# Kernel optimization log

Hardware: AMD Instinct MI355X
Metric: run time of the kernel (lower is better)

## Reference

```python
import jax, jax.numpy as jnp
import numpy as np
import math

D_MODEL = 1024
NUM_HEADS = 16
D_K = D_MODEL // NUM_HEADS
B, NQ, NK = 2, 2048, 2048


def setup_inputs() -> dict:
    key = jax.random.key(0)
    ks = jax.random.split(key, 14)
    s = 1.0 / math.sqrt(D_MODEL)
    inp = {
        "query": jax.random.normal(ks[0], (B, NQ, D_MODEL), jnp.float32),
        "key": jax.random.normal(ks[1], (B, NK, D_MODEL), jnp.float32),
        "value": jax.random.normal(ks[2], (B, NK, D_MODEL), jnp.float32),
        "mask": jax.random.randint(ks[3], (B, NK), 0, 2, jnp.int32),
        "attn_bias": jax.random.normal(ks[4], (B, NQ, NK), jnp.float32),
        "w_q": jax.random.normal(ks[5], (D_MODEL, D_MODEL), jnp.float32) * s,
        "b_q": jnp.zeros((D_MODEL,), jnp.float32),
        "w_k": jax.random.normal(ks[6], (D_MODEL, D_MODEL), jnp.float32) * s,
        "b_k": jnp.zeros((D_MODEL,), jnp.float32),
        "w_v": jax.random.normal(ks[7], (D_MODEL, D_MODEL), jnp.float32) * s,
        "b_v": jnp.zeros((D_MODEL,), jnp.float32),
        "w_o": jax.random.normal(ks[8], (D_MODEL, D_MODEL), jnp.float32) * s,
        "b_o": jnp.zeros((D_MODEL,), jnp.float32),
    }
    return inp


def reference(query, key, value, mask, attn_bias, w_q, b_q, w_k, b_k, w_v, b_v, w_o, b_o):
    # Linear projections (torch Linear: x @ W^T + b), reshape to [B, H, N, d_k]
    def proj(x, w, b, n):
        return (x @ w.T + b).reshape(x.shape[0], n, NUM_HEADS, D_K).transpose(0, 2, 1, 3)

    Q = proj(query, w_q, b_q, query.shape[1])   # [B,H,Nq,dk]
    K = proj(key, w_k, b_k, key.shape[1])       # [B,H,Nk,dk]
    V = proj(value, w_v, b_v, value.shape[1])   # [B,H,Nk,dk]

    scores = jnp.einsum("bhqd,bhkd->bhqk", Q, K) / math.sqrt(D_K)
    scores = scores + attn_bias[:, None, :, :]           # bias broadcast over heads
    pad = (mask[:, None, None, :] == 0)                   # [B,1,1,Nk]
    scores = jnp.where(pad, jnp.float32(-1e9), scores)
    attn = jax.nn.softmax(scores, axis=-1)                # dropout is identity (eval)
    out = jnp.einsum("bhqk,bhkd->bhqd", attn, V)          # [B,H,Nq,dk]
    out = out.transpose(0, 2, 1, 3).reshape(query.shape[0], query.shape[1], D_MODEL)
    return out @ w_o.T + b_o
```

## Files before the change

kernel.cpp:

```cpp
#include <hip/hip_runtime.h>


typedef short bf16x8 __attribute__((ext_vector_type(8)));
typedef short bf16x4 __attribute__((ext_vector_type(4)));
typedef float f32x4 __attribute__((ext_vector_type(4)));
typedef float f32x16 __attribute__((ext_vector_type(16)));
typedef int i32x4 __attribute__((ext_vector_type(4)));
typedef unsigned short u16;
typedef unsigned short u16x8 __attribute__((ext_vector_type(8)));
typedef unsigned short u16x4 __attribute__((ext_vector_type(4)));

#define MFMA16(a, b, c) __builtin_amdgcn_mfma_f32_16x16x32_bf16((a), (b), (c), 0, 0, 0)
#define MFMA32(a, b, c) __builtin_amdgcn_mfma_f32_32x32x16_bf16((a), (b), (c), 0, 0, 0)
#define GLD16(gp, lp)                                                     \
  __builtin_amdgcn_global_load_lds(                                       \
      (const __attribute__((address_space(1))) void*)(gp),                \
      (__attribute__((address_space(3))) void*)(lp), 16, 0, 0)

#define WAITVM_BAR(N) asm volatile("s_waitcnt vmcnt(" #N ")\ns_barrier" ::: "memory")
#define BAR() asm volatile("s_barrier" ::: "memory")

#if __has_builtin(__builtin_amdgcn_exp2f)
#define EXP2(x) __builtin_amdgcn_exp2f(x)
#else
#define EXP2(x) exp2f(x)
#endif

__device__ __forceinline__ u16 f2bf(float f) {
  union { float f; unsigned u; } v; v.f = f;
  return (u16)((v.u + 0x7fffu + ((v.u >> 16) & 1u)) >> 16);
}
__device__ __forceinline__ unsigned pk2(float x, float y) {
  union { float f; unsigned u; } a, b;
  a.f = x; b.f = y;
  return ((a.u + 0x8000u) >> 16) | ((b.u + 0x8000u) & 0xffff0000u);
}
__device__ __forceinline__ void pl32swap(unsigned& a, unsigned& b) {
  asm("v_permlane32_swap_b32 %0, %1" : "+v"(a), "+v"(b));
}

struct ConvDesc { const float* src; u16* dst; int n; };
struct ConvArgs { ConvDesc d[7]; };

__device__ __forceinline__ void biasprep_body(const float* __restrict__ bias,
                                              const int* __restrict__ mask,
                                              u16* __restrict__ out, int i) {
  const int o0 = i * 16;
  const int rowg = o0 >> 11;
  const int b = rowg >> 11;
  const int off = o0 & 2047;
  const int c = off >> 5;
  const int hi = (off >> 4) & 1;
  const float* src = bias + (size_t)rowg * 2048 + c * 32 + hi * 4;
  const int* msk = mask + b * 2048 + c * 32 + hi * 4;
  u16x8 w0 = {}, w1 = {};
#pragma unroll
  for (int t = 0; t < 4; t++) {
    f32x4 v = *(const f32x4*)(src + t * 8);
    i32x4 m = *(const i32x4*)(msk + t * 8);
#pragma unroll
    for (int j = 0; j < 4; j++) {
      u16 val = (m[j] != 0) ? f2bf(v[j] * 1.44269504f) : (u16)0xFF80;
      if (t < 2) w0[t * 4 + j] = val;
      else       w1[(t - 2) * 4 + j] = val;
    }
  }
  *(u16x8*)(out + o0) = w0;
  *(u16x8*)(out + o0 + 8) = w1;
}

__global__ __launch_bounds__(256)
void k_prep(ConvArgs a, const float* __restrict__ bias,
            const int* __restrict__ mask, u16* __restrict__ bout) {
  if (blockIdx.y == 7) {
    biasprep_body(bias, mask, bout, blockIdx.x * 256 + threadIdx.x);
    return;
  }
  ConvDesc cd = a.d[blockIdx.y];
  int i = (blockIdx.x * 256 + threadIdx.x) * 8;
  if (i >= cd.n) return;
  const float4* s = (const float4*)(cd.src + i);
  float4 f0 = s[0], f1 = s[1];
  u16x8 o;
  o[0] = f2bf(f0.x); o[1] = f2bf(f0.y); o[2] = f2bf(f0.z); o[3] = f2bf(f0.w);
  o[4] = f2bf(f1.x); o[5] = f2bf(f1.y); o[6] = f2bf(f1.z); o[7] = f2bf(f1.w);
  *(u16x8*)(cd.dst + i) = o;
}

__global__ __launch_bounds__(256)
void k_biasprep(const float* __restrict__ bias, const int* __restrict__ mask,
                u16* __restrict__ out) {
  biasprep_body(bias, mask, out, blockIdx.x * 256 + threadIdx.x);
}

template <int MF>
__device__ __forceinline__ void gemm_impl(const u16* __restrict__ A,
                                          const u16* __restrict__ Bw,
                                          const float* __restrict__ bias,
                                          void* __restrict__ outp, int mode,
                                          float oscale) {
  __shared__ u16 As[2][MF * 1024];
  __shared__ u16 Bs[2][4096];
  const int tid = threadIdx.x;
  const int lane = tid & 63;
  const int wv = tid >> 6;
  const int wr = wv >> 1, wc = wv & 1;
  const int m0 = blockIdx.y * (MF * 32), n0 = blockIdx.x * 128;

  f32x4 acc[MF][4] = {};

  const int s0 = tid, s1 = 256 + tid;
  const int r0 = s0 >> 2, c0 = (s0 & 3) ^ (r0 & 3);
  const int r1 = s1 >> 2, c1 = (s1 & 3) ^ (r1 & 3);
  const u16* gA0 = A + (size_t)(m0 + r0) * 1024 + c0 * 8;
  const u16* gA1 = A + (size_t)(m0 + r1) * 1024 + c1 * 8;
  const u16* gB0 = Bw + (size_t)(n0 + r0) * 1024 + c0 * 8;
  const u16* gB1 = Bw + (size_t)(n0 + r1) * 1024 + c1 * 8;
  u16* lA0 = &As[0][(tid & ~63) * 8];
  u16* lB0 = &Bs[0][(tid & ~63) * 8];

  GLD16(gA0, lA0);
  if constexpr (MF == 4) GLD16(gA1, lA0 + 2048);
  GLD16(gB0, lB0);
  GLD16(gB1, lB0 + 2048);
  WAITVM_BAR(0);

#define GSTEP(BUF, K0)                                                     \
  {                                                                        \
    const int nk = ((K0) + 32) & 1023;                                     \
    GLD16(gA0 + nk, lA0 + ((BUF) ^ 1) * (MF * 1024));                      \
    if constexpr (MF == 4)                                                 \
      GLD16(gA1 + nk, lA0 + 2048 + ((BUF) ^ 1) * (MF * 1024));             \
    GLD16(gB0 + nk, lB0 + ((BUF) ^ 1) * 4096);                             \
    GLD16(gB1 + nk, lB0 + 2048 + ((BUF) ^ 1) * 4096);                      \
    if constexpr (MF == 4) { WAITVM_BAR(4); } else { WAITVM_BAR(3); }      \
    bf16x8 af[MF], bfr[4];                                                 \
    _Pragma("unroll")                                                      \
    for (int mi = 0; mi < MF; mi++) {                                      \
      int row = wr * (MF * 16) + mi * 16 + (lane & 15);                    \
      int byt = row * 64 + (((lane >> 4) * 16) ^ ((row & 3) << 4));        \
      af[mi] = *(const bf16x8*)((const char*)&As[BUF][0] + byt);           \
    }                                                                      \
    _Pragma("unroll")                                                      \
    for (int ni = 0; ni < 4; ni++) {                                       \
      int row = wc * 64 + ni * 16 + (lane & 15);                           \
      int byt = row * 64 + (((lane >> 4) * 16) ^ ((row & 3) << 4));        \
      bfr[ni] = *(const bf16x8*)((const char*)&Bs[BUF][0] + byt);          \
    }                                                                      \
    __builtin_amdgcn_s_setprio(1);                                         \
    _Pragma("unroll")                                                      \
    for (int mi = 0; mi < MF; mi++)                                        \
      _Pragma("unroll")                                                    \
      for (int ni = 0; ni < 4; ni++)                                       \
        acc[mi][ni] = MFMA16(af[mi], bfr[ni], acc[mi][ni]);                \
    __builtin_amdgcn_s_setprio(0);                                         \
    BAR();                                                                 \
  }

  for (int k0 = 0; k0 < 1024; k0 += 64) {
    GSTEP(0, k0)
    GSTEP(1, k0 + 32)
  }
#undef GSTEP

#pragma unroll
  for (int ni = 0; ni < 4; ni++) {
    int n = n0 + wc * 64 + ni * 16 + (lane & 15);
    float bv = bias[n];
#pragma unroll
    for (int mi = 0; mi < MF; mi++) {
      int mb = m0 + wr * (MF * 16) + mi * 16 + (lane >> 4) * 4;
      if (mode == 2) {
        float* O = (float*)outp;
#pragma unroll
        for (int r = 0; r < 4; r++)
          O[(size_t)(mb + r) * 1024 + n] = (acc[mi][ni][r] + bv) * oscale;
      } else if (mode == 0) {
        u16* O = (u16*)outp;
        int b = mb >> 11, q = mb & 2047;
        int h = n >> 6, dk = n & 63;
        size_t base = ((size_t)(b * 16 + h) * 2048 + q) * 64 + dk;
#pragma unroll
        for (int r = 0; r < 4; r++)
          O[base + (size_t)r * 64] = f2bf((acc[mi][ni][r] + bv) * oscale);
      } else {
        u16* O = (u16*)outp;
        int b = mb >> 11, kv = mb & 2047;
        int h = n >> 6, dk = n & 63;
        u16x4 pk;
#pragma unroll
        for (int r = 0; r < 4; r++) pk[r] = f2bf((acc[mi][ni][r] + bv) * oscale);
        *(u16x4*)((u16*)O + ((size_t)((b * 16 + h) * 64 + dk)) * 2048 + kv) = pk;
      }
    }
  }
}

struct GemmDesc { const u16* A; const u16* W; const float* bias; void* out;
                  int mode; float oscale; };
struct Gemm3 { GemmDesc d[3]; };

__global__ __launch_bounds__(256, 2) void k_gemm_qkv(Gemm3 g3) {
  GemmDesc gd = g3.d[blockIdx.z];
  gemm_impl<4>(gd.A, gd.W, gd.bias, gd.out, gd.mode, gd.oscale);
}
__global__ __launch_bounds__(256, 2)
void k_gemm_o(const u16* __restrict__ A, const u16* __restrict__ W,
              const float* __restrict__ bias, float* __restrict__ out) {
  gemm_impl<2>(A, W, bias, out, 2, 1.0f);
}

__global__ __launch_bounds__(256, 2)
void k_attn(const u16* __restrict__ Qb, const u16* __restrict__ Kb,
            const u16* __restrict__ Vt, const u16* __restrict__ BiasE,
            u16* __restrict__ Ob) {
  __shared__ u16 Ks[2][128 * 64];
  __shared__ u16 Vs[2][64 * 128];

  const int tid = threadIdx.x, lane = tid & 63, w = tid >> 6;
  const int l31 = lane & 31, hi2 = lane >> 5;
  const int bid = blockIdx.x;
  const int xcd = bid & 7, rr = bid >> 3;
  const int qt = rr & 15;
  const int pr = xcd + 8 * (rr >> 4);
  const int b = pr >> 4, h = pr & 15;
  const int q0 = qt * 128;
  const size_t bh = (size_t)(b * 16 + h);

  const u16* Qrow = Qb + (bh * 2048 + q0 + w * 32 + l31) * 64 + hi2 * 8;
  bf16x8 bq[4];
#pragma unroll
  for (int dc = 0; dc < 4; dc++) bq[dc] = *(const bf16x8*)(Qrow + dc * 16);

  f32x16 acc[2] = {};
  float mrun = -1e30f, lrun = 0.f;

  const u16* Kg = Kb + bh * 2048 * 64;
  const u16* Vg = Vt + bh * 64 * 2048;
  int rK[4], cK[4], rV[4], cV[4], ldd[4];
#pragma unroll
  for (int i = 0; i < 4; i++) {
    int s = i * 256 + tid;
    rK[i] = s >> 3; cK[i] = (s & 7) ^ (rK[i] & 7);
    rV[i] = s >> 4; cV[i] = (s & 15) ^ (rV[i] & 7);
    ldd[i] = (i * 256 + (tid & ~63)) * 8;
  }
  const int kx = (lane & 7) << 4;

  const u16* brow =
      BiasE + ((size_t)b * 2048 + q0 + w * 32 + l31) * 2048 + hi2 * 16;

#pragma unroll
  for (int i = 0; i < 4; i++)
    GLD16(Kg + (size_t)rK[i] * 64 + cK[i] * 8, &Ks[0][ldd[i]]);
#pragma unroll
  for (int i = 0; i < 4; i++)
    GLD16(Vg + (size_t)rV[i] * 2048 + cV[i] * 8, &Vs[0][ldd[i]]);
  u16x8 bb[4][2];
#pragma unroll
  for (int c = 0; c < 4; c++) {
    bb[c][0] = *(const u16x8*)(brow + c * 32);
    bb[c][1] = *(const u16x8*)(brow + c * 32 + 8);
  }

#define ATTN_STEP(BUF, T)                                                      \
  {                                                                            \
    WAITVM_BAR(0);            \
    const char* kb = (const char*)&Ks[BUF][0];                                 \
    const char* vb = (const char*)&Vs[BUF][0];                                 \
    f32x16 sc[4];                                                              \
    __builtin_amdgcn_s_setprio(1);                                             \
    _Pragma("unroll")                                                          \
    for (int c = 0; c < 4; c++) {                                              \
      f32x16 z;                                                                \
      _Pragma("unroll")                                                        \
      for (int r = 0; r < 8; r++)                                              \
        z[r] = __uint_as_float((unsigned)bb[c][0][r] << 16);                   \
      _Pragma("unroll")                                                        \
      for (int r = 0; r < 8; r++)                                              \
        z[8 + r] = __uint_as_float((unsigned)bb[c][1][r] << 16);               \
      const int rowb = (c * 32 + l31) * 128;                                   \
      _Pragma("unroll")                                                        \
      for (int dc = 0; dc < 4; dc++) {                                         \
        bf16x8 ak =                                                            \
            *(const bf16x8*)(kb + rowb + ((dc * 32 + hi2 * 16) ^ kx));         \
        z = MFMA32(ak, bq[dc], z);                                             \
      }                                                                        \
      sc[c] = z;                                                               \
    }                                                                          \
    __builtin_amdgcn_s_setprio(0);                                             \
    const int nkv = (((T) + 1) & 15) * 128;                                    \
    _Pragma("unroll")                                                          \
    for (int i = 0; i < 4; i++)                                                \
      GLD16(Kg + (size_t)(nkv + rK[i]) * 64 + cK[i] * 8,                       \
            &Ks[(BUF) ^ 1][ldd[i]]);                                           \
    _Pragma("unroll")                                                          \
    for (int i = 0; i < 4; i++)                                                \
      GLD16(Vg + (size_t)rV[i] * 2048 + nkv + cV[i] * 8,                       \
            &Vs[(BUF) ^ 1][ldd[i]]);                                           \
    _Pragma("unroll")                                                          \
    for (int c = 0; c < 4; c++) {                                              \
      bb[c][0] = *(const u16x8*)(brow + nkv + c * 32);                         \
      bb[c][1] = *(const u16x8*)(brow + nkv + c * 32 + 8);                     \
    }                                                                          \
    float tmax = -3e38f;                                                       \
    _Pragma("unroll")                                                          \
    for (int c = 0; c < 4; c++)                                                \
      _Pragma("unroll")                                                        \
      for (int r = 0; r < 16; r++) tmax = fmaxf(tmax, sc[c][r]);               \
    tmax = fmaxf(tmax, __shfl_xor(tmax, 32, 64));                              \
    if (__any(tmax > mrun)) {                                                  \
      float mnew = fmaxf(mrun, tmax);                                          \
      float alpha = EXP2(mrun - mnew);                                         \
      mrun = mnew;                                                             \
      lrun *= alpha;                                                           \
      _Pragma("unroll")                                                        \
      for (int ds = 0; ds < 2; ds++)                                           \
        _Pragma("unroll")                                                      \
        for (int r = 0; r < 16; r++) acc[ds][r] *= alpha;                      \
    }                                                                          \
    float rsum = 0.f;                                                          \
    _Pragma("unroll")                                                          \
    for (int c = 0; c < 4; c++)                                                \
      _Pragma("unroll")                                                        \
      for (int r = 0; r < 16; r++) {                                           \
        sc[c][r] = EXP2(sc[c][r] - mrun);                                      \
        rsum += sc[c][r];                                                      \
      }                                                                        \
    rsum += __shfl_xor(rsum, 32, 64);                                          \
    lrun += rsum;                                                              \
    __builtin_amdgcn_s_setprio(1);                                             \
    _Pragma("unroll")                                                          \
    for (int c = 0; c < 4; c++) {                                              \
      unsigned a0 = pk2(sc[c][0], sc[c][1]), b0 = pk2(sc[c][4], sc[c][5]);     \
      unsigned a1 = pk2(sc[c][2], sc[c][3]), b1 = pk2(sc[c][6], sc[c][7]);     \
      unsigned e0 = pk2(sc[c][8], sc[c][9]), f0 = pk2(sc[c][12], sc[c][13]);   \
      unsigned e1 = pk2(sc[c][10], sc[c][11]), f1 = pk2(sc[c][14], sc[c][15]); \
      pl32swap(a0, b0); pl32swap(a1, b1);                                      \
      pl32swap(e0, f0); pl32swap(e1, f1);                                      \
      union { unsigned u[4]; bf16x8 v; } fe, fo;                               \
      fe.u[0] = a0; fe.u[1] = a1; fe.u[2] = b0; fe.u[3] = b1;                  \
      fo.u[0] = e0; fo.u[1] = e1; fo.u[2] = f0; fo.u[3] = f1;                  \
      _Pragma("unroll")                                                        \
      for (int ds = 0; ds < 2; ds++) {                                         \
        const int vrow = (ds * 32 + l31) * 256;                                \
        bf16x8 ve =                                                            \
            *(const bf16x8*)(vb + vrow + (((c * 4 + hi2) * 16) ^ kx));         \
        acc[ds] = MFMA32(ve, fe.v, acc[ds]);                                   \
        bf16x8 vo =                                                            \
            *(const bf16x8*)(vb + vrow + (((c * 4 + 2 + hi2) * 16) ^ kx));     \
        acc[ds] = MFMA32(vo, fo.v, acc[ds]);                                   \
      }                                                                        \
    }                                                                          \
    __builtin_amdgcn_s_setprio(0);                                             \
  }

  for (int t = 0; t < 16; t += 2) {
    ATTN_STEP(0, t)
    ATTN_STEP(1, t + 1)
  }
#undef ATTN_STEP

  float linv = 1.0f / lrun;
  const size_t obase =
      ((size_t)b * 2048 + q0 + w * 32 + l31) * 1024 + h * 64 + hi2 * 4;
#pragma unroll
  for (int ds = 0; ds < 2; ds++)
#pragma unroll
    for (int t = 0; t < 4; t++) {
      u16x4 pk;
#pragma unroll
      for (int j = 0; j < 4; j++) pk[j] = f2bf(acc[ds][t * 4 + j] * linv);
      *(u16x4*)(Ob + obase + ds * 32 + t * 8) = pk;
    }
}

extern "C" void kernel_launch(void* const* d_in, const int* in_sizes, int n_in,
                              void* d_out, int out_size, void* d_ws,
                              size_t ws_size, hipStream_t stream) {
  (void)in_sizes; (void)n_in; (void)out_size;
  const float* q_in = (const float*)d_in[0];
  const float* k_in = (const float*)d_in[1];
  const float* v_in = (const float*)d_in[2];
  const int* mask = (const int*)d_in[3];
  const float* attn_bias = (const float*)d_in[4];
  const float* w_q = (const float*)d_in[5];
  const float* b_q = (const float*)d_in[6];
  const float* w_k = (const float*)d_in[7];
  const float* b_k = (const float*)d_in[8];
  const float* w_v = (const float*)d_in[9];
  const float* b_v = (const float*)d_in[10];
  const float* w_o = (const float*)d_in[11];
  const float* b_o = (const float*)d_in[12];

  const size_t MB = 1u << 20;
  char* ws = (char*)d_ws;
  u16* XQ = (u16*)(ws + 0 * MB);
  u16* XK = (u16*)(ws + 8 * MB);
  u16* XV = (u16*)(ws + 16 * MB);
  u16* WQ = (u16*)(ws + 24 * MB);
  u16* WK = (u16*)(ws + 26 * MB);
  u16* WV = (u16*)(ws + 28 * MB);
  u16* WO = (u16*)(ws + 30 * MB);
  u16* Qb = (u16*)(ws + 32 * MB);
  u16* Kb = (u16*)(ws + 40 * MB);
  u16* Vt = (u16*)(ws + 48 * MB);
  u16* Ob = (u16*)(ws + 56 * MB);
  const bool merged = ws_size >= (size_t)80 * MB;
  u16* BiasE = (u16*)(ws + (merged ? 64 : 0) * MB);

  ConvArgs ca;
  ca.d[0] = {q_in, XQ, 4096 * 1024};
  ca.d[1] = {k_in, XK, 4096 * 1024};
  ca.d[2] = {v_in, XV, 4096 * 1024};
  ca.d[3] = {w_q, WQ, 1024 * 1024};
  ca.d[4] = {w_k, WK, 1024 * 1024};
  ca.d[5] = {w_v, WV, 1024 * 1024};
  ca.d[6] = {w_o, WO, 1024 * 1024};
  k_prep<<<dim3(2048, merged ? 8 : 7), 256, 0, stream>>>(ca, attn_bias, mask,
                                                         BiasE);

  const float QSCALE = 0.125f * 1.44269504f;
  Gemm3 g3;
  g3.d[0] = {XQ, WQ, b_q, (void*)Qb, 0, QSCALE};
  g3.d[1] = {XK, WK, b_k, (void*)Kb, 0, 1.0f};
  g3.d[2] = {XV, WV, b_v, (void*)Vt, 1, 1.0f};
  k_gemm_qkv<<<dim3(8, 32, 3), 256, 0, stream>>>(g3);

  if (!merged) k_biasprep<<<2048, 256, 0, stream>>>(attn_bias, mask, BiasE);

  k_attn<<<512, 256, 0, stream>>>(Qb, Kb, Vt, BiasE, Ob);

  k_gemm_o<<<dim3(8, 64), 256, 0, stream>>>(Ob, WO, b_o, (float*)d_out);
}
```

Before: 149.3 us.

## Software-pipeline attention so P·V of previous tile overlaps next QK^T

Restructures the attention loop so each step first issues the QK^T MFMAs for the current tile, then the P·V MFMAs for the previous tile's probabilities. Those probabilities are kept in registers and read from the other V buffer, with an epilogue that drains the last tile. The aim is to hide the softmax dependency chain behind matrix work and to skip the wasted prefetch on the final tile. The step adds a barrier before prefetch to protect the V buffer still in use. It also turns the max and sum reductions into trees and raises the QKV GEMM occupancy hint to 3 blocks, both of which add register pressure.

```diff
diff --git a/kernel.cpp b/kernel.cpp
--- a/kernel.cpp
+++ b/kernel.cpp
@@ -200,7 +200,7 @@
                   int mode; float oscale; };
 struct Gemm3 { GemmDesc d[3]; };
 
-__global__ __launch_bounds__(256, 2) void k_gemm_qkv(Gemm3 g3) {
+__global__ __launch_bounds__(256, 3) void k_gemm_qkv(Gemm3 g3) {
   GemmDesc gd = g3.d[blockIdx.z];
   gemm_impl<4>(gd.A, gd.W, gd.bias, gd.out, gd.mode, gd.oscale);
 }
@@ -235,6 +235,9 @@
   f32x16 acc[2] = {};
   float mrun = -1e30f, lrun = 0.f;
 
+  union PF { unsigned u[4]; bf16x8 v; };
+  PF pfe[4], pfo[4];
+
   const u16* Kg = Kb + bh * 2048 * 64;
   const u16* Vg = Vt + bh * 64 * 2048;
   int rK[4], cK[4], rV[4], cV[4], ldd[4];
@@ -263,11 +266,11 @@
     bb[c][1] = *(const u16x8*)(brow + c * 32 + 8);
   }
 
-#define ATTN_STEP(BUF, T)                                                      \
+#define ATTN_STEP(BUF, T, HASPV)                                               \
   {                                                                            \
-    WAITVM_BAR(0);            \
+    WAITVM_BAR(0);      \
     const char* kb = (const char*)&Ks[BUF][0];                                 \
-    const char* vb = (const char*)&Vs[BUF][0];                                 \
+    const char* vprev = (const char*)&Vs[(BUF) ^ 1][0];                        \
     f32x16 sc[4];                                                              \
     __builtin_amdgcn_s_setprio(1);                                             \
     _Pragma("unroll")                                                          \
@@ -288,26 +291,51 @@
       }                                                                        \
       sc[c] = z;                                                               \
     }                                                                          \
+    if (HASPV) {                                                               \
+      _Pragma("unroll")                                                        \
+      for (int c = 0; c < 4; c++) {                                            \
+        _Pragma("unroll")                                                      \
+        for (int ds = 0; ds < 2; ds++) {                                       \
+          const int vrow = (ds * 32 + l31) * 256;                              \
+          bf16x8 ve =                                                          \
+              *(const bf16x8*)(vprev + vrow + (((c * 4 + hi2) * 16) ^ kx));    \
+          acc[ds] = MFMA32(ve, pfe[c].v, acc[ds]);                             \
+          bf16x8 vo =                                                          \
+              *(const bf16x8*)(vprev + vrow + (((c * 4 + 2 + hi2) * 16) ^ kx)); \
+          acc[ds] = MFMA32(vo, pfo[c].v, acc[ds]);                             \
+        }                                                                      \
+      }                                                                        \
+    }                                                                          \
     __builtin_amdgcn_s_setprio(0);                                             \
-    const int nkv = (((T) + 1) & 15) * 128;                                    \
-    _Pragma("unroll")                                                          \
-    for (int i = 0; i < 4; i++)                                                \
-      GLD16(Kg + (size_t)(nkv + rK[i]) * 64 + cK[i] * 8,                       \
-            &Ks[(BUF) ^ 1][ldd[i]]);                                           \
-    _Pragma("unroll")                                                          \
-    for (int i = 0; i < 4; i++)                                                \
-      GLD16(Vg + (size_t)rV[i] * 2048 + nkv + cV[i] * 8,                       \
-            &Vs[(BUF) ^ 1][ldd[i]]);                                           \
+    BAR();      \
+    if ((T) + 1 < 16) {  \
+      const int nkv = ((T) + 1) * 128;                                         \
+      _Pragma("unroll")                                                        \
+      for (int i = 0; i < 4; i++)                                              \
+        GLD16(Kg + (size_t)(nkv + rK[i]) * 64 + cK[i] * 8,                     \
+              &Ks[(BUF) ^ 1][ldd[i]]);                                         \
+      _Pragma("unroll")                                                        \
+      for (int i = 0; i < 4; i++)                                              \
+        GLD16(Vg + (size_t)rV[i] * 2048 + nkv + cV[i] * 8,                     \
+              &Vs[(BUF) ^ 1][ldd[i]]);                                         \
+      _Pragma("unroll")                                                        \
+      for (int c = 0; c < 4; c++) {                                            \
+        bb[c][0] = *(const u16x8*)(brow + nkv + c * 32);                       \
+        bb[c][1] = *(const u16x8*)(brow + nkv + c * 32 + 8);                   \
+      }                                                                        \
+    }                                                                          \
+    float cm[4];                                                               \
     _Pragma("unroll")                                                          \
     for (int c = 0; c < 4; c++) {                                              \
-      bb[c][0] = *(const u16x8*)(brow + nkv + c * 32);                         \
-      bb[c][1] = *(const u16x8*)(brow + nkv + c * 32 + 8);                     \
-    }                                                                          \
-    float tmax = -3e38f;                                                       \
-    _Pragma("unroll")                                                          \
-    for (int c = 0; c < 4; c++)                                                \
-      _Pragma("unroll")                                                        \
-      for (int r = 0; r < 16; r++) tmax = fmaxf(tmax, sc[c][r]);               \
+      float t8[8];                                                             \
+      _Pragma("unroll")                                                        \
+      for (int r = 0; r < 8; r++) t8[r] = fmaxf(sc[c][r], sc[c][r + 8]);       \
+      float t4[4];                                                             \
+      _Pragma("unroll")                                                        \
+      for (int r = 0; r < 4; r++) t4[r] = fmaxf(t8[r], t8[r + 4]);             \
+      cm[c] = fmaxf(fmaxf(t4[0], t4[1]), fmaxf(t4[2], t4[3]));                 \
+    }                                                                          \
+    float tmax = fmaxf(fmaxf(cm[0], cm[1]), fmaxf(cm[2], cm[3]));              \
     tmax = fmaxf(tmax, __shfl_xor(tmax, 32, 64));                              \
     if (__any(tmax > mrun)) {                                                  \
       float mnew = fmaxf(mrun, tmax);                                          \
@@ -319,17 +347,24 @@
         _Pragma("unroll")                                                      \
         for (int r = 0; r < 16; r++) acc[ds][r] *= alpha;                      \
     }                                                                          \
-    float rsum = 0.f;                                                          \
     _Pragma("unroll")                                                          \
     for (int c = 0; c < 4; c++)                                                \
       _Pragma("unroll")                                                        \
-      for (int r = 0; r < 16; r++) {                                           \
-        sc[c][r] = EXP2(sc[c][r] - mrun);                                      \
-        rsum += sc[c][r];                                                      \
-      }                                                                        \
+      for (int r = 0; r < 16; r++) sc[c][r] = EXP2(sc[c][r] - mrun);           \
+    float cs[4];                                                               \
+    _Pragma("unroll")                                                          \
+    for (int c = 0; c < 4; c++) {                                              \
+      float s8[8];                                                             \
+      _Pragma("unroll")                                                        \
+      for (int r = 0; r < 8; r++) s8[r] = sc[c][r] + sc[c][r + 8];             \
+      float s4[4];                                                             \
+      _Pragma("unroll")                                                        \
+      for (int r = 0; r < 4; r++) s4[r] = s8[r] + s8[r + 4];                   \
+      cs[c] = (s4[0] + s4[1]) + (s4[2] + s4[3]);                               \
+    }                                                                          \
+    float rsum = (cs[0] + cs[1]) + (cs[2] + cs[3]);                            \
     rsum += __shfl_xor(rsum, 32, 64);                                          \
     lrun += rsum;                                                              \
-    __builtin_amdgcn_s_setprio(1);                                             \
     _Pragma("unroll")                                                          \
     for (int c = 0; c < 4; c++) {                                              \
       unsigned a0 = pk2(sc[c][0], sc[c][1]), b0 = pk2(sc[c][4], sc[c][5]);     \
@@ -338,28 +373,35 @@
       unsigned e1 = pk2(sc[c][10], sc[c][11]), f1 = pk2(sc[c][14], sc[c][15]); \
       pl32swap(a0, b0); pl32swap(a1, b1);                                      \
       pl32swap(e0, f0); pl32swap(e1, f1);                                      \
-      union { unsigned u[4]; bf16x8 v; } fe, fo;                               \
-      fe.u[0] = a0; fe.u[1] = a1; fe.u[2] = b0; fe.u[3] = b1;                  \
-      fo.u[0] = e0; fo.u[1] = e1; fo.u[2] = f0; fo.u[3] = f1;                  \
-      _Pragma("unroll")                                                        \
-      for (int ds = 0; ds < 2; ds++) {                                         \
-        const int vrow = (ds * 32 + l31) * 256;                                \
-        bf16x8 ve =                                                            \
-            *(const bf16x8*)(vb + vrow + (((c * 4 + hi2) * 16) ^ kx));         \
-        acc[ds] = MFMA32(ve, fe.v, acc[ds]);                                   \
-        bf16x8 vo =                                                            \
-            *(const bf16x8*)(vb + vrow + (((c * 4 + 2 + hi2) * 16) ^ kx));     \
-        acc[ds] = MFMA32(vo, fo.v, acc[ds]);                                   \
-      }                                                                        \
-    }                                                                          \
-    __builtin_amdgcn_s_setprio(0);                                             \
-  }
-
-  for (int t = 0; t < 16; t += 2) {
-    ATTN_STEP(0, t)
-    ATTN_STEP(1, t + 1)
+      pfe[c].u[0] = a0; pfe[c].u[1] = a1; pfe[c].u[2] = b0; pfe[c].u[3] = b1;  \
+      pfo[c].u[0] = e0; pfo[c].u[1] = e1; pfo[c].u[2] = f0; pfo[c].u[3] = f1;  \
+    }                                                                          \
+  }
+
+  ATTN_STEP(0, 0, 0)
+  ATTN_STEP(1, 1, 1)
+  for (int t = 2; t < 16; t += 2) {
+    ATTN_STEP(0, t, 1)
+    ATTN_STEP(1, t + 1, 1)
   }
 #undef ATTN_STEP
+
+  {
+    const char* vprev = (const char*)&Vs[1][0];
+#pragma unroll
+    for (int c = 0; c < 4; c++) {
+#pragma unroll
+      for (int ds = 0; ds < 2; ds++) {
+        const int vrow = (ds * 32 + l31) * 256;
+        bf16x8 ve =
+            *(const bf16x8*)(vprev + vrow + (((c * 4 + hi2) * 16) ^ kx));
+        acc[ds] = MFMA32(ve, pfe[c].v, acc[ds]);
+        bf16x8 vo =
+            *(const bf16x8*)(vprev + vrow + (((c * 4 + 2 + hi2) * 16) ^ kx));
+        acc[ds] = MFMA32(vo, pfo[c].v, acc[ds]);
+      }
+    }
+  }
 
   float linv = 1.0f / lrun;
   const size_t obase =
```

Result: no change. 152.2 us (+2.0%).

## Split attention KV range across wave pairs with smaller tiles and merge partials

Applied to the files above, without the earlier changes.

The attention kernel now processes 64 query rows per block, with two wave pairs each covering half of the KV sequence (split-K), and merges their partial softmax states through LDS at the end. KV tiles shrink to 32 columns, with a double-buffered K tile and a triple-buffered V tile, and the grid doubles to 1024 blocks. Launch bounds are raised to target 4 blocks per CU for attention and 3 for the QKV GEMM, and online-softmax rescaling is skipped unless the max grows by more than 8. This aims to raise occupancy and latency hiding, at the cost of more barriers per KV element, a cross-wave reduction, and register pressure under the tighter launch bounds.

```diff
diff --git a/kernel.cpp b/kernel.cpp
--- a/kernel.cpp
+++ b/kernel.cpp
@@ -200,7 +200,7 @@
                   int mode; float oscale; };
 struct Gemm3 { GemmDesc d[3]; };
 
-__global__ __launch_bounds__(256, 2) void k_gemm_qkv(Gemm3 g3) {
+__global__ __launch_bounds__(256, 3) void k_gemm_qkv(Gemm3 g3) {
   GemmDesc gd = g3.d[blockIdx.z];
   gemm_impl<4>(gd.A, gd.W, gd.bias, gd.out, gd.mode, gd.oscale);
 }
@@ -210,24 +210,27 @@
   gemm_impl<2>(A, W, bias, out, 2, 1.0f);
 }
 
-__global__ __launch_bounds__(256, 2)
+__global__ __launch_bounds__(256, 4)
 void k_attn(const u16* __restrict__ Qb, const u16* __restrict__ Kb,
             const u16* __restrict__ Vt, const u16* __restrict__ BiasE,
             u16* __restrict__ Ob) {
-  __shared__ u16 Ks[2][128 * 64];
-  __shared__ u16 Vs[2][64 * 128];
+  __shared__ __attribute__((aligned(16))) char LB[40960];
 
   const int tid = threadIdx.x, lane = tid & 63, w = tid >> 6;
   const int l31 = lane & 31, hi2 = lane >> 5;
+  const int qg = w & 1, sp = w >> 1;
   const int bid = blockIdx.x;
   const int xcd = bid & 7, rr = bid >> 3;
-  const int qt = rr & 15;
-  const int pr = xcd + 8 * (rr >> 4);
+  const int qt = rr & 31;
+  const int pr = xcd + 8 * (rr >> 5);
   const int b = pr >> 4, h = pr & 15;
-  const int q0 = qt * 128;
+  const int q0 = qt * 64;
   const size_t bh = (size_t)(b * 16 + h);
-
-  const u16* Qrow = Qb + (bh * 2048 + q0 + w * 32 + l31) * 64 + hi2 * 8;
+  const int kvb = sp * 1024;
+
+  char* spb = LB + sp * 20480;
+
+  const u16* Qrow = Qb + (bh * 2048 + q0 + qg * 32 + l31) * 64 + hi2 * 8;
   bf16x8 bq[4];
 #pragma unroll
   for (int dc = 0; dc < 4; dc++) bq[dc] = *(const bf16x8*)(Qrow + dc * 16);
@@ -237,142 +240,144 @@
 
   const u16* Kg = Kb + bh * 2048 * 64;
   const u16* Vg = Vt + bh * 64 * 2048;
-  int rK[4], cK[4], rV[4], cV[4], ldd[4];
-#pragma unroll
-  for (int i = 0; i < 4; i++) {
-    int s = i * 256 + tid;
-    rK[i] = s >> 3; cK[i] = (s & 7) ^ (rK[i] & 7);
-    rV[i] = s >> 4; cV[i] = (s & 15) ^ (rV[i] & 7);
-    ldd[i] = (i * 256 + (tid & ~63)) * 8;
-  }
+
+  const int s0 = qg * 64 + lane, s1 = s0 + 128;
+  const int rK0 = s0 >> 3, cK0 = (s0 & 7) ^ (rK0 & 7);
+  const int rK1 = s1 >> 3, cK1 = (s1 & 7) ^ (rK1 & 7);
+  const int rV0 = s0 >> 2, cV0 = (s0 & 3) ^ (rV0 & 3);
+  const int rV1 = s1 >> 2, cV1 = (s1 & 3) ^ (rV1 & 3);
+  const int kdo = qg * 1024;
   const int kx = (lane & 7) << 4;
+  const int kxv = (lane & 3) << 4;
 
   const u16* brow =
-      BiasE + ((size_t)b * 2048 + q0 + w * 32 + l31) * 2048 + hi2 * 16;
-
-#pragma unroll
-  for (int i = 0; i < 4; i++)
-    GLD16(Kg + (size_t)rK[i] * 64 + cK[i] * 8, &Ks[0][ldd[i]]);
-#pragma unroll
-  for (int i = 0; i < 4; i++)
-    GLD16(Vg + (size_t)rV[i] * 2048 + cV[i] * 8, &Vs[0][ldd[i]]);
-  u16x8 bb[4][2];
-#pragma unroll
-  for (int c = 0; c < 4; c++) {
-    bb[c][0] = *(const u16x8*)(brow + c * 32);
-    bb[c][1] = *(const u16x8*)(brow + c * 32 + 8);
-  }
-
-#define ATTN_STEP(BUF, T)                                                      \
-  {                                                                            \
-    WAITVM_BAR(0);            \
-    const char* kb = (const char*)&Ks[BUF][0];                                 \
-    const char* vb = (const char*)&Vs[BUF][0];                                 \
-    f32x16 sc[4];                                                              \
-    __builtin_amdgcn_s_setprio(1);                                             \
-    _Pragma("unroll")                                                          \
-    for (int c = 0; c < 4; c++) {                                              \
-      f32x16 z;                                                                \
-      _Pragma("unroll")                                                        \
-      for (int r = 0; r < 8; r++)                                              \
-        z[r] = __uint_as_float((unsigned)bb[c][0][r] << 16);                   \
-      _Pragma("unroll")                                                        \
-      for (int r = 0; r < 8; r++)                                              \
-        z[8 + r] = __uint_as_float((unsigned)bb[c][1][r] << 16);               \
-      const int rowb = (c * 32 + l31) * 128;                                   \
-      _Pragma("unroll")                                                        \
-      for (int dc = 0; dc < 4; dc++) {                                         \
-        bf16x8 ak =                                                            \
-            *(const bf16x8*)(kb + rowb + ((dc * 32 + hi2 * 16) ^ kx));         \
-        z = MFMA32(ak, bq[dc], z);                                             \
-      }                                                                        \
-      sc[c] = z;                                                               \
-    }                                                                          \
-    __builtin_amdgcn_s_setprio(0);                                             \
-    const int nkv = (((T) + 1) & 15) * 128;                                    \
-    _Pragma("unroll")                                                          \
-    for (int i = 0; i < 4; i++)                                                \
-      GLD16(Kg + (size_t)(nkv + rK[i]) * 64 + cK[i] * 8,                       \
-            &Ks[(BUF) ^ 1][ldd[i]]);                                           \
-    _Pragma("unroll")                                                          \
-    for (int i = 0; i < 4; i++)                                                \
-      GLD16(Vg + (size_t)rV[i] * 2048 + nkv + cV[i] * 8,                       \
-            &Vs[(BUF) ^ 1][ldd[i]]);                                           \
-    _Pragma("unroll")                                                          \
-    for (int c = 0; c < 4; c++) {                                              \
-      bb[c][0] = *(const u16x8*)(brow + nkv + c * 32);                         \
-      bb[c][1] = *(const u16x8*)(brow + nkv + c * 32 + 8);                     \
-    }                                                                          \
-    float tmax = -3e38f;                                                       \
-    _Pragma("unroll")                                                          \
-    for (int c = 0; c < 4; c++)                                                \
-      _Pragma("unroll")                                                        \
-      for (int r = 0; r < 16; r++) tmax = fmaxf(tmax, sc[c][r]);               \
-    tmax = fmaxf(tmax, __shfl_xor(tmax, 32, 64));                              \
-    if (__any(tmax > mrun)) {                                                  \
-      float mnew = fmaxf(mrun, tmax);                                          \
-      float alpha = EXP2(mrun - mnew);                                         \
-      mrun = mnew;                                                             \
-      lrun *= alpha;                                                           \
-      _Pragma("unroll")                                                        \
-      for (int ds = 0; ds < 2; ds++)                                           \
-        _Pragma("unroll")                                                      \
-        for (int r = 0; r < 16; r++) acc[ds][r] *= alpha;                      \
-    }                                                                          \
-    float rsum = 0.f;                                                          \
-    _Pragma("unroll")                                                          \
-    for (int c = 0; c < 4; c++)                                                \
-      _Pragma("unroll")                                                        \
-      for (int r = 0; r < 16; r++) {                                           \
-        sc[c][r] = EXP2(sc[c][r] - mrun);                                      \
-        rsum += sc[c][r];                                                      \
-      }                                                                        \
-    rsum += __shfl_xor(rsum, 32, 64);                                          \
-    lrun += rsum;                                                              \
-    __builtin_amdgcn_s_setprio(1);                                             \
-    _Pragma("unroll")                                                          \
-    for (int c = 0; c < 4; c++) {                                              \
-      unsigned a0 = pk2(sc[c][0], sc[c][1]), b0 = pk2(sc[c][4], sc[c][5]);     \
-      unsigned a1 = pk2(sc[c][2], sc[c][3]), b1 = pk2(sc[c][6], sc[c][7]);     \
-      unsigned e0 = pk2(sc[c][8], sc[c][9]), f0 = pk2(sc[c][12], sc[c][13]);   \
-      unsigned e1 = pk2(sc[c][10], sc[c][11]), f1 = pk2(sc[c][14], sc[c][15]); \
-      pl32swap(a0, b0); pl32swap(a1, b1);                                      \
-      pl32swap(e0, f0); pl32swap(e1, f1);                                      \
-      union { unsigned u[4]; bf16x8 v; } fe, fo;                               \
-      fe.u[0] = a0; fe.u[1] = a1; fe.u[2] = b0; fe.u[3] = b1;                  \
-      fo.u[0] = e0; fo.u[1] = e1; fo.u[2] = f0; fo.u[3] = f1;                  \
-      _Pragma("unroll")                                                        \
-      for (int ds = 0; ds < 2; ds++) {                                         \
-        const int vrow = (ds * 32 + l31) * 256;                                \
-        bf16x8 ve =                                                            \
-            *(const bf16x8*)(vb + vrow + (((c * 4 + hi2) * 16) ^ kx));         \
-        acc[ds] = MFMA32(ve, fe.v, acc[ds]);                                   \
-        bf16x8 vo =                                                            \
-            *(const bf16x8*)(vb + vrow + (((c * 4 + 2 + hi2) * 16) ^ kx));     \
-        acc[ds] = MFMA32(vo, fo.v, acc[ds]);                                   \
-      }                                                                        \
-    }                                                                          \
-    __builtin_amdgcn_s_setprio(0);                                             \
-  }
-
-  for (int t = 0; t < 16; t += 2) {
-    ATTN_STEP(0, t)
-    ATTN_STEP(1, t + 1)
-  }
-#undef ATTN_STEP
-
-  float linv = 1.0f / lrun;
-  const size_t obase =
-      ((size_t)b * 2048 + q0 + w * 32 + l31) * 1024 + h * 64 + hi2 * 4;
-#pragma unroll
-  for (int ds = 0; ds < 2; ds++)
-#pragma unroll
-    for (int t = 0; t < 4; t++) {
-      u16x4 pk;
-#pragma unroll
-      for (int j = 0; j < 4; j++) pk[j] = f2bf(acc[ds][t * 4 + j] * linv);
-      *(u16x4*)(Ob + obase + ds * 32 + t * 8) = pk;
-    }
+      BiasE + ((size_t)b * 2048 + q0 + qg * 32 + l31) * 2048 + hi2 * 16;
+
+  u16x8 bb0 = *(const u16x8*)(brow + kvb);
+  u16x8 bb1 = *(const u16x8*)(brow + kvb + 8);
+  GLD16(Kg + (size_t)(kvb + rK0) * 64 + cK0 * 8, spb + kdo);
+  GLD16(Kg + (size_t)(kvb + rK1) * 64 + cK1 * 8, spb + kdo + 2048);
+  GLD16(Vg + (size_t)rV0 * 2048 + kvb + cV0 * 8, spb + 8192 + kdo);
+  GLD16(Vg + (size_t)rV1 * 2048 + kvb + cV1 * 8, spb + 8192 + kdo + 2048);
+
+#pragma unroll
+  for (int T = 0; T < 32; ++T) {
+    WAITVM_BAR(0);
+    const char* kb = spb + (T & 1) * 4096;
+    const char* vb = spb + 8192 + (T % 3) * 4096;
+
+    f32x16 z;
+#pragma unroll
+    for (int r = 0; r < 8; r++)
+      z[r] = __uint_as_float((unsigned)bb0[r] << 16);
+#pragma unroll
+    for (int r = 0; r < 8; r++)
+      z[8 + r] = __uint_as_float((unsigned)bb1[r] << 16);
+    __builtin_amdgcn_s_setprio(1);
+#pragma unroll
+    for (int dc = 0; dc < 4; dc++) {
+      bf16x8 ak =
+          *(const bf16x8*)(kb + l31 * 128 + ((dc * 32 + hi2 * 16) ^ kx));
+      z = MFMA32(ak, bq[dc], z);
+    }
+    __builtin_amdgcn_s_setprio(0);
+
+    if (T < 31) {
+      const int nkv = kvb + (T + 1) * 32;
+      bb0 = *(const u16x8*)(brow + nkv);
+      bb1 = *(const u16x8*)(brow + nkv + 8);
+      char* kd = spb + (((T + 1) & 1)) * 4096 + kdo;
+      GLD16(Kg + (size_t)(nkv + rK0) * 64 + cK0 * 8, kd);
+      GLD16(Kg + (size_t)(nkv + rK1) * 64 + cK1 * 8, kd + 2048);
+      char* vd = spb + 8192 + ((T + 1) % 3) * 4096 + kdo;
+      GLD16(Vg + (size_t)rV0 * 2048 + nkv + cV0 * 8, vd);
+      GLD16(Vg + (size_t)rV1 * 2048 + nkv + cV1 * 8, vd + 2048);
+    }
+
+    float m8[8];
+#pragma unroll
+    for (int r = 0; r < 8; r++) m8[r] = fmaxf(z[r], z[r + 8]);
+    float tmax = fmaxf(fmaxf(fmaxf(m8[0], m8[1]), fmaxf(m8[2], m8[3])),
+                       fmaxf(fmaxf(m8[4], m8[5]), fmaxf(m8[6], m8[7])));
+    tmax = fmaxf(tmax, __shfl_xor(tmax, 32, 64));
+    if (__any(tmax > mrun + 8.f)) {
+      float mnew = fmaxf(mrun, tmax);
+      float alpha = EXP2(mrun - mnew);
+      mrun = mnew;
+      lrun *= alpha;
+#pragma unroll
+      for (int ds = 0; ds < 2; ds++)
+#pragma unroll
+        for (int r = 0; r < 16; r++) acc[ds][r] *= alpha;
+    }
+#pragma unroll
+    for (int r = 0; r < 16; r++) z[r] = EXP2(z[r] - mrun);
+    float s8[8];
+#pragma unroll
+    for (int r = 0; r < 8; r++) s8[r] = z[r] + z[r + 8];
+    float rsum = ((s8[0] + s8[1]) + (s8[2] + s8[3])) +
+                 ((s8[4] + s8[5]) + (s8[6] + s8[7]));
+    lrun += rsum + __shfl_xor(rsum, 32, 64);
+
+    union PF { unsigned u[4]; bf16x8 v; } pfe, pfo;
+    {
+      unsigned a0 = pk2(z[0], z[1]), b0v = pk2(z[4], z[5]);
+      unsigned a1 = pk2(z[2], z[3]), b1v = pk2(z[6], z[7]);
+      unsigned e0 = pk2(z[8], z[9]), f0v = pk2(z[12], z[13]);
+      unsigned e1 = pk2(z[10], z[11]), f1v = pk2(z[14], z[15]);
+      pl32swap(a0, b0v); pl32swap(a1, b1v);
+      pl32swap(e0, f0v); pl32swap(e1, f1v);
+      pfe.u[0] = a0; pfe.u[1] = a1; pfe.u[2] = b0v; pfe.u[3] = b1v;
+      pfo.u[0] = e0; pfo.u[1] = e1; pfo.u[2] = f0v; pfo.u[3] = f1v;
+    }
+
+    __builtin_amdgcn_s_setprio(1);
+#pragma unroll
+    for (int ds = 0; ds < 2; ds++) {
+      const int vrow = (ds * 32 + l31) * 64;
+      bf16x8 ve = *(const bf16x8*)(vb + vrow + ((hi2 * 16) ^ kxv));
+      acc[ds] = MFMA32(ve, pfe.v, acc[ds]);
+      bf16x8 vo = *(const bf16x8*)(vb + vrow + (((2 + hi2) * 16) ^ kxv));
+      acc[ds] = MFMA32(vo, pfo.v, acc[ds]);
+    }
+    __builtin_amdgcn_s_setprio(0);
+  }
+
+  __syncthreads();
+  char* cb = LB + 20480 + qg * 8704;
+  if (sp == 1) {
+#pragma unroll
+    for (int ds = 0; ds < 2; ds++)
+#pragma unroll
+      for (int r4 = 0; r4 < 4; r4++) {
+        float4 v = make_float4(acc[ds][r4 * 4 + 0], acc[ds][r4 * 4 + 1],
+                               acc[ds][r4 * 4 + 2], acc[ds][r4 * 4 + 3]);
+        *(float4*)(cb + ds * 4096 + r4 * 1024 + lane * 16) = v;
+      }
+    *(float2*)(cb + 8192 + lane * 8) = make_float2(mrun, lrun);
+  }
+  __syncthreads();
+  if (sp == 0) {
+    float2 ml1 = *(const float2*)(cb + 8192 + lane * 8);
+    float M = fmaxf(mrun, ml1.x);
+    float a0 = EXP2(mrun - M), a1 = EXP2(ml1.x - M);
+    float linv = 1.0f / (a0 * lrun + a1 * ml1.y);
+    a0 *= linv; a1 *= linv;
+    const size_t obase =
+        ((size_t)b * 2048 + q0 + qg * 32 + l31) * 1024 + h * 64 + hi2 * 4;
+#pragma unroll
+    for (int ds = 0; ds < 2; ds++)
+#pragma unroll
+      for (int t = 0; t < 4; t++) {
+        float4 p1 = *(const float4*)(cb + ds * 4096 + t * 1024 + lane * 16);
+        u16x4 pk;
+        pk[0] = f2bf(a0 * acc[ds][t * 4 + 0] + a1 * p1.x);
+        pk[1] = f2bf(a0 * acc[ds][t * 4 + 1] + a1 * p1.y);
+        pk[2] = f2bf(a0 * acc[ds][t * 4 + 2] + a1 * p1.z);
+        pk[3] = f2bf(a0 * acc[ds][t * 4 + 3] + a1 * p1.w);
+        *(u16x4*)(Ob + obase + ds * 32 + t * 8) = pk;
+      }
+  }
 }
 
 extern "C" void kernel_launch(void* const* d_in, const int* in_sizes, int n_in,
@@ -429,7 +434,7 @@
 
   if (!merged) k_biasprep<<<2048, 256, 0, stream>>>(attn_bias, mask, BiasE);
 
-  k_attn<<<512, 256, 0, stream>>>(Qb, Kb, Vt, BiasE, Ob);
+  k_attn<<<1024, 256, 0, stream>>>(Qb, Kb, Vt, BiasE, Ob);
 
   k_gemm_o<<<dim3(8, 64), 256, 0, stream>>>(Ob, WO, b_o, (float*)d_out);
 }
```

After: 159.0 us. 6.5% more time.
